# Kernel optimization log

Hardware: AMD Instinct MI355X
Metric: run time of the kernel (lower is better)

## Reference

```python
import jax, jax.numpy as jnp
import numpy as np


def setup_inputs() -> dict:
    key = jax.random.key(0)
    k1, k2 = jax.random.split(key)
    B, C, H, W = 4, 64, 256, 256
    x = jax.random.normal(k1, (B, C, H, W), dtype=jnp.float32)
    perspective = jax.random.uniform(k2, (B, 1, H, W), dtype=jnp.float32)
    alpha = jnp.ones((1,), dtype=jnp.float32) * 3.0   # sigma scale
    beta = jnp.ones((1,), dtype=jnp.float32)          # sigmoid slope
    gamma = jnp.zeros((1,), dtype=jnp.float32)        # sigmoid shift
    return {"x": x, "perspective": perspective, "alpha": alpha,
            "beta": beta, "gamma": gamma, "kernel_size": 7}


def reference(x, perspective, alpha, beta, gamma, kernel_size):
    K = int(kernel_size)
    pad = K // 2
    B, C, H, W = x.shape
    # AdaptiveSigmoid sigma map, clamped like the torch module
    sigma = jnp.maximum(alpha * jax.nn.sigmoid(beta * perspective + gamma), 1e-4)  # [B,1,H,W]
    inv2s2 = 1.0 / (2.0 * sigma * sigma)                                           # [B,1,H,W]
    # squared distance of each kernel tap from center (static)
    offs = np.arange(K) - pad
    d2 = (offs[:, None] ** 2 + offs[None, :] ** 2).reshape(-1).astype(np.float32)  # [K*K]
    # per-pixel, per-tap Gaussian weights, normalized over taps
    w = jnp.exp(-d2[:, None, None, None, None] * inv2s2[None])  # [K*K,B,1,H,W]
    w = w / jnp.sum(w, axis=0)
    xp = jnp.pad(x, ((0, 0), (0, 0), (pad, pad), (pad, pad)))
    out = jnp.zeros_like(x)
    k = 0
    for i in range(K):            # fixed small K*K loop (49 taps), jit-friendly
        for j in range(K):
            out = out + w[k] * xp[:, :, i:i + H, j:j + W]
            k += 1
    return out
```

## Files before the change

### kernel.cpp

```cpp
#include <hip/hip_runtime.h>

#define NB 4
#define NC 64
#define NH 256
#define NW 256
#define TH 32
#define SROWS (TH + 6)
#define LROW 264

__global__ __launch_bounds__(256)
void wprep(const float* __restrict__ persp,
           const float* __restrict__ alpha_p,
           const float* __restrict__ beta_p,
           const float* __restrict__ gamma_p,
           float* __restrict__ wg)
{
    const float alpha = alpha_p[0];
    const float beta  = beta_p[0];
    const float gamma = gamma_p[0];
    const int i = (blockIdx.x * 256 + threadIdx.x) * 4;
    const float4 p = *(const float4*)(persp + i);
    const float pa[4] = {p.x, p.y, p.z, p.w};
    float g[4];
    #pragma unroll
    for (int k = 0; k < 4; ++k) {
        const float z  = fmaf(beta, pa[k], gamma);
        const float sg = __builtin_amdgcn_rcpf(1.0f + __expf(-z));
        const float sigma = fmaxf(alpha * sg, 1e-4f);
        const float t  = 0.5f * __builtin_amdgcn_rcpf(sigma * sigma);
        g[k] = __expf(-t);
    }
    *(float4*)(wg + i) = make_float4(g[0], g[1], g[2], g[3]);
}

__global__ __launch_bounds__(256, 3)
void adaptive_gauss7(const float* __restrict__ x,
                     const float* __restrict__ wgp,
                     float* __restrict__ out)
{
    __shared__ float lds[SROWS * LROW];

    const int tid  = threadIdx.x;
    const int lane = tid & 63;
    const int wv   = tid >> 6;
    const int c    = blockIdx.x;
    const int h0   = blockIdx.y * TH;
    const int b    = blockIdx.z;
    const int colbase = lane * 4;
    const int rg      = h0 + wv * 8;

    const float* xc   = x   + (size_t)(b * NC + c) * NH * NW;
    float*       outp = out + (size_t)(b * NC + c) * NH * NW;
    const float* wrow = wgp + (size_t)b * NH * NW;

    float4 wsg[8];
    #pragma unroll
    for (int o = 0; o < 8; ++o)
        wsg[o] = *(const float4*)(wrow + (size_t)(rg + o) * NW + colbase);

    if (tid < SROWS) {
        *(float4*)&lds[tid * LROW]       = make_float4(0.f, 0.f, 0.f, 0.f);
        *(float4*)&lds[tid * LROW + 260] = make_float4(0.f, 0.f, 0.f, 0.f);
    }

    for (int r = wv; r < SROWS; r += 4) {
        const int gr = h0 - 3 + r;
        if ((unsigned)gr < NH) {
            __builtin_amdgcn_global_load_lds(
                (const __attribute__((address_space(1))) void*)(xc + (size_t)gr * NW + colbase),
                (__attribute__((address_space(3))) void*)&lds[r * LROW + 4],
                16, 0, 0);
        } else {
            *(float4*)&lds[r * LROW + 4 + colbase] = make_float4(0.f, 0.f, 0.f, 0.f);
        }
    }
    __syncthreads();

    float win[7][10];
    auto fill = [&](float (&dst)[10], int tr) {
        const float* rp = &lds[tr * LROW + colbase];
        const float4 a0 = *(const float4*)(rp);
        const float4 a1 = *(const float4*)(rp + 4);
        const float4 a2 = *(const float4*)(rp + 8);
        dst[0] = a0.y; dst[1] = a0.z; dst[2] = a0.w;
        dst[3] = a1.x; dst[4] = a1.y; dst[5] = a1.z; dst[6] = a1.w;
        dst[7] = a2.x; dst[8] = a2.y; dst[9] = a2.z;
    };
    #pragma unroll
    for (int r = 0; r < 7; ++r)
        fill(win[r], wv * 8 + r);

    #pragma unroll
    for (int o = 0; o < 8; ++o) {
        const float gk[4] = {wsg[o].x, wsg[o].y, wsg[o].z, wsg[o].w};
        float res[4];
        #pragma unroll
        for (int k = 0; k < 4; ++k) {
            const float g  = gk[k];
            const float g2 = g * g;
            const float p4 = g2 * g2;
            const float p9 = p4 * p4 * g;
            const float S  = fmaf(2.0f, (g + p4) + p9, 1.0f);
            const float inv  = __builtin_amdgcn_rcpf(S);
            const float inv2 = inv * inv;

            float rs[7];
            #pragma unroll
            for (int j = 0; j < 7; ++j) {
                const int s = (o + j) % 7;
                rs[j] = fmaf(p9, win[s][k]     + win[s][k + 6],
                        fmaf(p4, win[s][k + 1] + win[s][k + 5],
                        fmaf(g,  win[s][k + 2] + win[s][k + 4],
                                 win[s][k + 3])));
            }
            const float acc = fmaf(p9, rs[0] + rs[6],
                              fmaf(p4, rs[1] + rs[5],
                              fmaf(g,  rs[2] + rs[4],
                                       rs[3])));
            res[k] = acc * inv2;
        }
        *(float4*)(outp + (size_t)(rg + o) * NW + colbase) =
            make_float4(res[0], res[1], res[2], res[3]);

        if (o < 7)
            fill(win[o % 7], wv * 8 + o + 7);
    }
}

extern "C" void kernel_launch(void* const* d_in, const int* in_sizes, int n_in,
                              void* d_out, int out_size, void* d_ws, size_t ws_size,
                              hipStream_t stream) {
    const float* x     = (const float*)d_in[0];
    const float* persp = (const float*)d_in[1];
    const float* alpha = (const float*)d_in[2];
    const float* beta  = (const float*)d_in[3];
    const float* gamma = (const float*)d_in[4];
    float* outp        = (float*)d_out;
    float* wg          = (float*)d_ws;

    wprep<<<dim3((NB * NH * NW) / 1024), dim3(256), 0, stream>>>(persp, alpha, beta, gamma, wg);
    adaptive_gauss7<<<dim3(NC, NH / TH, NB), dim3(256), 0, stream>>>(x, wg, outp);
}
```

Before: 140.2 us.

## Replace LDS halo reads with DPP cross-lane shifts for horizontal neighbors

Drops the padded LDS row layout, so each thread loads only its own four columns per row. The three left and right neighbour values come from adjacent lanes through DPP wave shift-by-one, whose bound_ctrl zero fill stands in for the image-border padding. The vertical accumulation is also regrouped into symmetric partial sums. This reduces LDS traffic and register pressure, at the cost of extra DPP instructions that depend on wave-wide shift semantics being available.

```diff
diff --git a/kernel.cpp b/kernel.cpp
--- a/kernel.cpp
+++ b/kernel.cpp
@@ -6,7 +6,7 @@
 #define NW 256
 #define TH 32
 #define SROWS (TH + 6)
-#define LROW 264
+#define LROW 256
 
 __global__ __launch_bounds__(256)
 void wprep(const float* __restrict__ persp,
@@ -31,6 +31,15 @@
         g[k] = __expf(-t);
     }
     *(float4*)(wg + i) = make_float4(g[0], g[1], g[2], g[3]);
+}
+
+__device__ __forceinline__ float dpp_shr1(float v) {
+    return __int_as_float(__builtin_amdgcn_update_dpp(
+        0, __float_as_int(v), 0x138 , 0xf, 0xf, true));
+}
+__device__ __forceinline__ float dpp_shl1(float v) {
+    return __int_as_float(__builtin_amdgcn_update_dpp(
+        0, __float_as_int(v), 0x130 , 0xf, 0xf, true));
 }
 
 __global__ __launch_bounds__(256, 3)
@@ -58,72 +67,85 @@
     for (int o = 0; o < 8; ++o)
         wsg[o] = *(const float4*)(wrow + (size_t)(rg + o) * NW + colbase);
 
-    if (tid < SROWS) {
-        *(float4*)&lds[tid * LROW]       = make_float4(0.f, 0.f, 0.f, 0.f);
-        *(float4*)&lds[tid * LROW + 260] = make_float4(0.f, 0.f, 0.f, 0.f);
-    }
-
     for (int r = wv; r < SROWS; r += 4) {
         const int gr = h0 - 3 + r;
         if ((unsigned)gr < NH) {
             __builtin_amdgcn_global_load_lds(
                 (const __attribute__((address_space(1))) void*)(xc + (size_t)gr * NW + colbase),
-                (__attribute__((address_space(3))) void*)&lds[r * LROW + 4],
+                (__attribute__((address_space(3))) void*)&lds[r * LROW],
                 16, 0, 0);
         } else {
-            *(float4*)&lds[r * LROW + 4 + colbase] = make_float4(0.f, 0.f, 0.f, 0.f);
+            *(float4*)&lds[r * LROW + colbase] = make_float4(0.f, 0.f, 0.f, 0.f);
         }
     }
     __syncthreads();
 
-    float win[7][10];
-    auto fill = [&](float (&dst)[10], int tr) {
-        const float* rp = &lds[tr * LROW + colbase];
-        const float4 a0 = *(const float4*)(rp);
-        const float4 a1 = *(const float4*)(rp + 4);
-        const float4 a2 = *(const float4*)(rp + 8);
-        dst[0] = a0.y; dst[1] = a0.z; dst[2] = a0.w;
-        dst[3] = a1.x; dst[4] = a1.y; dst[5] = a1.z; dst[6] = a1.w;
-        dst[7] = a2.x; dst[8] = a2.y; dst[9] = a2.z;
-    };
+    float win[7][4];
     #pragma unroll
-    for (int r = 0; r < 7; ++r)
-        fill(win[r], wv * 8 + r);
+    for (int r = 0; r < 7; ++r) {
+        const float4 a = *(const float4*)&lds[(wv * 8 + r) * LROW + colbase];
+        win[r][0] = a.x; win[r][1] = a.y; win[r][2] = a.z; win[r][3] = a.w;
+    }
 
     #pragma unroll
     for (int o = 0; o < 8; ++o) {
         const float gk[4] = {wsg[o].x, wsg[o].y, wsg[o].z, wsg[o].w};
+        float g[4], p4[4], p9[4], inv2[4];
+        #pragma unroll
+        for (int k = 0; k < 4; ++k) {
+            g[k] = gk[k];
+            const float g2 = g[k] * g[k];
+            p4[k] = g2 * g2;
+            p9[k] = p4[k] * p4[k] * g[k];
+            const float S  = fmaf(2.0f, (g[k] + p4[k]) + p9[k], 1.0f);
+            const float iv = __builtin_amdgcn_rcpf(S);
+            inv2[k] = iv * iv;
+        }
+
+        float s0[4], s1[4], s2[4], s3[4];
+        #pragma unroll
+        for (int j = 0; j < 7; ++j) {
+            const int s = (o + j) % 7;
+            const float w[10] = {
+                dpp_shr1(win[s][1]),
+                dpp_shr1(win[s][2]),
+                dpp_shr1(win[s][3]),
+                win[s][0], win[s][1], win[s][2], win[s][3],
+                dpp_shl1(win[s][0]),
+                dpp_shl1(win[s][1]),
+                dpp_shl1(win[s][2])
+            };
+            #pragma unroll
+            for (int k = 0; k < 4; ++k) {
+                const float rs = fmaf(p9[k], w[k]     + w[k + 6],
+                                 fmaf(p4[k], w[k + 1] + w[k + 5],
+                                 fmaf(g[k],  w[k + 2] + w[k + 4],
+                                             w[k + 3])));
+                if      (j == 0) s0[k] = rs;
+                else if (j == 1) s1[k] = rs;
+                else if (j == 2) s2[k] = rs;
+                else if (j == 3) s3[k] = rs;
+                else if (j == 4) s2[k] = s2[k] + rs;
+                else if (j == 5) s1[k] = s1[k] + rs;
+                else             s0[k] = s0[k] + rs;
+            }
+        }
+
         float res[4];
         #pragma unroll
         for (int k = 0; k < 4; ++k) {
-            const float g  = gk[k];
-            const float g2 = g * g;
-            const float p4 = g2 * g2;
-            const float p9 = p4 * p4 * g;
-            const float S  = fmaf(2.0f, (g + p4) + p9, 1.0f);
-            const float inv  = __builtin_amdgcn_rcpf(S);
-            const float inv2 = inv * inv;
-
-            float rs[7];
-            #pragma unroll
-            for (int j = 0; j < 7; ++j) {
-                const int s = (o + j) % 7;
-                rs[j] = fmaf(p9, win[s][k]     + win[s][k + 6],
-                        fmaf(p4, win[s][k + 1] + win[s][k + 5],
-                        fmaf(g,  win[s][k + 2] + win[s][k + 4],
-                                 win[s][k + 3])));
-            }
-            const float acc = fmaf(p9, rs[0] + rs[6],
-                              fmaf(p4, rs[1] + rs[5],
-                              fmaf(g,  rs[2] + rs[4],
-                                       rs[3])));
-            res[k] = acc * inv2;
+            res[k] = fmaf(p9[k], s0[k],
+                     fmaf(p4[k], s1[k],
+                     fmaf(g[k],  s2[k], s3[k]))) * inv2[k];
         }
         *(float4*)(outp + (size_t)(rg + o) * NW + colbase) =
             make_float4(res[0], res[1], res[2], res[3]);
 
-        if (o < 7)
-            fill(win[o % 7], wv * 8 + o + 7);
+        if (o < 7) {
+            const float4 a = *(const float4*)&lds[(wv * 8 + o + 7) * LROW + colbase];
+            win[o % 7][0] = a.x; win[o % 7][1] = a.y;
+            win[o % 7][2] = a.z; win[o % 7][3] = a.w;
+        }
     }
 }
 
```

Measured after the change: 136.1 us. 3.0% less time.
